# Optimization experiments

Measured on AMD Instinct MI355X. Metric: run time of the kernel, lower is better.

## Reference

```python
import jax, jax.numpy as jnp
import numpy as np
import jax.scipy.linalg as jsl

# dims
B, DIN = 4096, 256      # data
OUT, M = 32, 128        # output GPs, inducing points
NH = 2                  # hyperparameter samples
JITTER = 1e-4


def vec2tril(vec, m):
    """Fill lower-triangular (row-major) from packed vector."""
    i, j = jnp.tril_indices(m)
    out = jnp.zeros(vec.shape[:-1] + (m, m), vec.dtype)
    return out.at[..., i, j].set(vec)


def _hypers(theta):
    sf2 = jnp.exp(theta[:, 0])        # (NH,) signal variance
    ls = jnp.exp(theta[:, 1:])        # (NH, DIN) ARD lengthscales
    return sf2, ls


def kernel_zz(theta, z):
    """RBF K(z,z): (NH, OUT, M, M)."""
    sf2, ls = _hypers(theta)
    zs = z[None] / ls[:, None, None, :]              # (NH, OUT, M, DIN)
    n2 = (zs ** 2).sum(-1)                           # (NH, OUT, M)
    cross = jnp.einsum('homd,hond->homn', zs, zs)
    d2 = jnp.maximum(n2[..., :, None] + n2[..., None, :] - 2.0 * cross, 0.0)
    return sf2[:, None, None, None] * jnp.exp(-0.5 * d2)


def kernel_zx(theta, z, x):
    """RBF K(z,x): (NH, OUT, M, B)."""
    sf2, ls = _hypers(theta)
    zs = z[None] / ls[:, None, None, :]              # (NH, OUT, M, DIN)
    xs = x[None] / ls[:, None, :]                    # (NH, B, DIN)
    z2 = (zs ** 2).sum(-1)                           # (NH, OUT, M)
    x2 = (xs ** 2).sum(-1)                           # (NH, B)
    cross = jnp.einsum('homd,hbd->homb', zs, xs)     # (NH, OUT, M, B)
    d2 = jnp.maximum(z2[..., None] + x2[:, None, None, :] - 2.0 * cross, 0.0)
    return sf2[:, None, None, None] * jnp.exp(-0.5 * d2)


def setup_inputs() -> dict:
    key = jax.random.key(0)
    k1, k2, k3, k4, k5 = jax.random.split(key, 5)
    x = jax.random.normal(k1, (B, DIN), jnp.float32)
    z = jax.random.normal(k2, (OUT, M, DIN), jnp.float32)
    u_mean = jax.random.normal(k3, (OUT, M, 1), jnp.float32) * 0.5
    u_tril_vec = jax.random.uniform(k4, (OUT, M * (M + 1) // 2), jnp.float32)
    theta = jax.random.normal(k5, (NH, 1 + DIN), jnp.float32)
    return {"x": x, "z": z, "u_mean": u_mean, "u_tril_vec": u_tril_vec, "theta": theta}


def reference(x, z, u_mean, u_tril_vec, theta):
    m = z.shape[-2]
    u_tril = vec2tril(u_tril_vec, m)                        # (OUT, M, M)

    kuf = kernel_zx(theta, z, x)                            # (NH, OUT, M, B)
    kuu = kernel_zz(theta, z)                               # (NH, OUT, M, M)
    Lkuu = jnp.linalg.cholesky(kuu + JITTER * jnp.eye(m, dtype=kuu.dtype))

    bshape = Lkuu.shape[:-2]
    u_mean_b = jnp.broadcast_to(u_mean, bshape + u_mean.shape[-2:])
    u_tril_b = jnp.broadcast_to(u_tril, bshape + u_tril.shape[-2:])

    LKinvu = jsl.solve_triangular(Lkuu, u_mean_b, lower=True)   # (NH, OUT, M, 1)
    LKinvKuf = jsl.solve_triangular(Lkuu, kuf, lower=True)      # (NH, OUT, M, B)

    sf2, _ = _hypers(theta)
    kff_diag = sf2[:, None, None]                               # (NH, 1, 1)

    diag1 = (LKinvKuf ** 2).sum(-2)                             # (NH, OUT, B)
    LKinvLs = jsl.solve_triangular(Lkuu, u_tril_b, lower=True)  # (NH, OUT, M, M)
    vec2 = jnp.einsum('...ij,...ik->...jk', LKinvLs, LKinvKuf)  # (NH, OUT, M, B)
    diag2 = (vec2 ** 2).sum(-2)                                 # (NH, OUT, B)

    mu = jnp.einsum('...ij,...ik->...jk', LKinvKuf, LKinvu)[..., 0]  # (NH, OUT, B)
    var = kff_diag - diag1 + diag2                                   # (NH, OUT, B)
    return mu, var
```

## Files before the change

kernel.cpp:

```cpp
#include <hip/hip_runtime.h>
#include <cstdint>
#include <cstddef>

constexpr int B_   = 4096;
constexpr int DIN  = 256;
constexpr int OUT_ = 32;
constexpr int MM   = 128;
constexpr int NH_  = 2;
constexpr int HO   = 64;
constexpr int TRIL = 8256;
constexpr float JIT = 1e-4f;

constexpr size_t al4k(size_t x){ return (x + 4095) & ~size_t(4095); }
constexpr size_t OFF_FLAG  = 0;
constexpr size_t OFF_INVLS = 4096;
constexpr size_t OFF_SF2   = al4k(OFF_INVLS + 2*256*4);
constexpr size_t OFF_ZN2   = al4k(OFF_SF2 + 64);
constexpr size_t OFF_XN2   = al4k(OFF_ZN2 + 8192*4);
constexpr size_t OFF_W     = al4k(OFF_XN2 + 8192*4);
constexpr size_t OFF_ZS    = al4k(OFF_W + 8192*4);
constexpr size_t OFF_XS    = al4k(OFF_ZS + (size_t)2097152*2);
constexpr size_t OFF_VTH   = al4k(OFF_XS + (size_t)2097152*2);
constexpr size_t OFF_VTL   = al4k(OFF_VTH + (size_t)1048576*2);
constexpr size_t OFF_CHI   = al4k(OFF_VTL + (size_t)1048576*2);
constexpr size_t OFF_CLO   = al4k(OFF_CHI + (size_t)1048576*2);

typedef float f32x4 __attribute__((ext_vector_type(4)));
typedef short short8 __attribute__((ext_vector_type(8)));

__device__ __forceinline__ float bf2f(unsigned short u){
  union{unsigned int i; float f;} v; v.i = ((unsigned)u) << 16; return v.f;
}
__device__ __forceinline__ unsigned short f2bf(float f){
  union{float f; unsigned int i;} v; v.f = f;
  unsigned int r = v.i + 0x7fffu + ((v.i >> 16) & 1u);
  return (unsigned short)(r >> 16);
}
__device__ __forceinline__ float ldin(const void* p, size_t i, int isbf){
  if (isbf) return bf2f(((const unsigned short*)p)[i]);
  return ((const float*)p)[i];
}
__device__ __forceinline__ void stout(void* p, size_t i, float v, int isbf){
  if (isbf) ((unsigned short*)p)[i] = f2bf(v);
  else ((float*)p)[i] = v;
}
__device__ __forceinline__ void gl_lds16(const unsigned short* g, unsigned short* l){
  __builtin_amdgcn_global_load_lds(
      (const __attribute__((address_space(1))) unsigned int*)g,
      (__attribute__((address_space(3))) unsigned int*)l, 16, 0, 0);
}

__global__ void k_hypers(const void* __restrict__ theta, const void* __restrict__ x,
                         int* __restrict__ flagp,
                         float* __restrict__ inv_ls, float* __restrict__ sf2){
  __shared__ int sflag;
  int t = threadIdx.x;
  if (t < 64){
    unsigned int w0 = ((const unsigned int*)theta)[t];
    unsigned int w1 = ((const unsigned int*)x)[t];
    float a0 = fabsf(bf2f((unsigned short)(w0 & 0xffffu)));
    float a1 = fabsf(bf2f((unsigned short)(w1 & 0xffffu)));
    int c = ((a0 > 9.3e-10f && a0 < 64.f) ? 1 : 0) + ((a1 > 9.3e-10f && a1 < 64.f) ? 1 : 0);
    c += __shfl_down(c, 32); c += __shfl_down(c, 16); c += __shfl_down(c, 8);
    c += __shfl_down(c, 4);  c += __shfl_down(c, 2);  c += __shfl_down(c, 1);
    if (t == 0){ sflag = (c >= 64) ? 1 : 0; *flagp = sflag; }
  }
  __syncthreads();
  const int isbf = sflag;
  for (int i = t; i < NH_*257; i += blockDim.x){
    int h = i / 257, j = i - h*257;
    float v = ldin(theta, i, isbf);
    if (j == 0) sf2[h] = __expf(v);
    else inv_ls[h*DIN + j - 1] = __expf(-v);
  }
}

__global__ void k_scale(const void* __restrict__ xsrc, const void* __restrict__ zsrc,
                        const int* flagp, const float* __restrict__ inv_ls,
                        unsigned short* __restrict__ xdst, unsigned short* __restrict__ zdst,
                        float* __restrict__ xn2, float* __restrict__ zn2){
  const int isbf = *flagp;
  const int wave = threadIdx.x >> 6, lane = threadIdx.x & 63;
  int bx = blockIdx.x;
  const void* src; unsigned short* dst; float* n2; int r;
  if (bx < 1024){ src = xsrc; dst = xdst; n2 = xn2; r = bx*4 + wave; }
  else          { src = zsrc; dst = zdst; n2 = zn2; r = (bx-1024)*4 + wave; }
  const int d0 = lane*4;
  float v[4];
  if (isbf){
    uint2 uu = *(const uint2*)((const unsigned short*)src + (size_t)r*DIN + d0);
    v[0]=bf2f((unsigned short)(uu.x & 0xffffu)); v[1]=bf2f((unsigned short)(uu.x >> 16));
    v[2]=bf2f((unsigned short)(uu.y & 0xffffu)); v[3]=bf2f((unsigned short)(uu.y >> 16));
  } else {
    f32x4 f = *(const f32x4*)((const float*)src + (size_t)r*DIN + d0);
    v[0]=f[0]; v[1]=f[1]; v[2]=f[2]; v[3]=f[3];
  }
  #pragma unroll
  for (int h = 0; h < 2; ++h){
    f32x4 il = *(const f32x4*)(inv_ls + h*DIN + d0);
    unsigned short rb[4];
    float p = 0.f;
    #pragma unroll
    for (int k = 0; k < 4; ++k){
      float s = v[k] * il[k];
      rb[k] = f2bf(s);
      float qv = bf2f(rb[k]);
      p += qv*qv;
    }
    uint2 pk;
    pk.x = (unsigned)rb[0] | ((unsigned)rb[1] << 16);
    pk.y = (unsigned)rb[2] | ((unsigned)rb[3] << 16);
    *(uint2*)(dst + ((size_t)h*4096 + r)*DIN + d0) = pk;
    p += __shfl_xor(p, 32); p += __shfl_xor(p, 16); p += __shfl_xor(p, 8);
    p += __shfl_xor(p, 4);  p += __shfl_xor(p, 2);  p += __shfl_xor(p, 1);
    if (lane == 0) n2[(size_t)h*4096 + r] = p;
  }
}

constexpr int TLD = 20;
constexpr int TSZ = 16*TLD;
__device__ __forceinline__ int tb(int bi, int bj){ return (bi*(bi+1)/2 + bj)*TSZ; }
__device__ __forceinline__ int vb(int bi, int bj){ return (36 + bi*(bi-1)/2 + bj)*TSZ; }
__device__ __forceinline__ int tri_bi(int t){
  int bi = (int)((sqrtf(8.f*t + 1.f) - 1.f) * 0.5f);
  while ((bi+1)*(bi+2)/2 <= t) ++bi;
  while (bi*(bi+1)/2 > t) --bi;
  return bi;
}

__global__ __launch_bounds__(256) void k_kufact(
    const unsigned short* __restrict__ zs, const float* __restrict__ zn2,
    const float* __restrict__ sf2,
    unsigned short* __restrict__ VTh, unsigned short* __restrict__ VTl){
  const int ho = blockIdx.x, h = ho >> 5;
  const int tid = threadIdx.x;
  const int lane = tid & 63, wid = tid >> 6;
  const int l15 = lane & 15, q = lane >> 4;
  const int wn = wid * 32;
  extern __shared__ float T[];
  unsigned short* zsl = (unsigned short*)T;
  float* zn2l = T + 64*TSZ;
  if (tid < 128) zn2l[tid] = zn2[ho*128 + tid];
  const size_t zbase = (size_t)ho * 32768;
  const int sw = ((q ^ ((l15 >> 1) & 3)) << 3);
  const f32x4 z4 = {0.f,0.f,0.f,0.f};
  f32x4 acc[8][2];
  #pragma unroll
  for (int mt=0; mt<8; ++mt){ acc[mt][0]=z4; acc[mt][1]=z4; }
  for (int kc = 0; kc < 8; ++kc){
    __syncthreads();
    {
      int rA = wn + (lane >> 2);
      int sg = ((lane & 3) ^ ((rA >> 1) & 3)) << 3;
      gl_lds16(zs + zbase + (size_t)rA*256 + kc*32 + sg, zsl + wn*32);
      gl_lds16(zs + zbase + (size_t)(rA+16)*256 + kc*32 + sg, zsl + (wn+16)*32);
    }
    __syncthreads();
    short8 b0 = *(const short8*)(zsl + (wn      + l15)*32 + sw);
    short8 b1 = *(const short8*)(zsl + (wn + 16 + l15)*32 + sw);
    #pragma unroll
    for (int mt=0; mt<8; ++mt){
      short8 a = *(const short8*)(zsl + (mt*16 + l15)*32 + sw);
      acc[mt][0] = __builtin_amdgcn_mfma_f32_16x16x32_bf16(a, b0, acc[mt][0], 0,0,0);
      acc[mt][1] = __builtin_amdgcn_mfma_f32_16x16x32_bf16(a, b1, acc[mt][1], 0,0,0);
    }
  }
  __syncthreads();
  const float s2v = sf2[h];
  #pragma unroll
  for (int nt=0; nt<2; ++nt){
    int n = wn + nt*16 + l15;
    float nn = zn2l[n];
    int bn = n >> 4;
    #pragma unroll
    for (int mt=0; mt<8; ++mt){
      #pragma unroll
      for (int r=0; r<4; ++r){
        int m = mt*16 + q*4 + r;
        float d2 = fmaxf(zn2l[m] + nn - 2.f*acc[mt][nt][r], 0.f);
        float a = s2v * __expf(-0.5f*d2);
        if (m == n) a += JIT;
        int bm = m >> 4;
        if (bn <= bm) T[tb(bm, bn) + (m & 15)*TLD + (n & 15)] = a;
      }
    }
  }
  __syncthreads();
  for (int kb = 0; kb < 8; ++kb){
    if (wid == 0){
      float* D = T + tb(kb, kb);
      const int r = lane & 15;
      const bool act = (lane < 16);
      float a[16];
      #pragma unroll
      for (int k = 0; k < 16; ++k) a[k] = 0.f;
      if (act){
        #pragma unroll
        for (int k2 = 0; k2 < 4; ++k2)
          *(f32x4*)(a + 4*k2) = *(const f32x4*)(D + r*TLD + 4*k2);
      }
      #pragma unroll
      for (int c = 0; c < 16; ++c){
        float pr[16];
        #pragma unroll
        for (int k = 0; k < 16; ++k) pr[k] = __shfl(a[k], c);
        float rsq = rsqrtf(pr[c]);
        if (act && r >= c) a[c] *= rsq;
        float lrc = a[c];
        #pragma unroll
        for (int k = 0; k < 16; ++k)
          if (k > c && act && r > c) a[k] -= lrc * (pr[k] * rsq);
      }
      float v[16];
      #pragma unroll
      for (int k = 0; k < 16; ++k) v[k] = 0.f;
      const int c = lane & 15;
      #pragma unroll
      for (int i = 0; i < 16; ++i){
        float lrow[16];
        #pragma unroll
        for (int k = 0; k < 16; ++k) lrow[k] = __shfl(a[k], i);
        float rli = 1.f / lrow[i];
        float s = 0.f;
        #pragma unroll
        for (int k = 0; k < 16; ++k)
          if (k < i) s += ((k >= c) ? lrow[k]*v[k] : 0.f);
        v[i] = (c == i) ? rli : ((c < i) ? -s*rli : 0.f);
      }
      if (act){
        #pragma unroll
        for (int i = 0; i < 16; ++i) D[i*TLD + c] = v[i];
      }
    }
    __syncthreads();
    {
      const int gi = kb*16 + 16 + tid;
      if (gi < 128){
        float* Bp = T + tb(gi >> 4, kb) + (gi & 15)*TLD;
        const float* Vd = T + tb(kb, kb);
        float b[16], nb[16];
        #pragma unroll
        for (int k2 = 0; k2 < 4; ++k2) *(f32x4*)(b + 4*k2) = *(const f32x4*)(Bp + 4*k2);
        #pragma unroll
        for (int j = 0; j < 16; ++j){
          float s = 0.f;
          #pragma unroll
          for (int k = 0; k < 16; ++k)
            if (k <= j) s += b[k] * Vd[j*TLD + k];
          nb[j] = s;
        }
        #pragma unroll
        for (int k2 = 0; k2 < 4; ++k2) *(f32x4*)(Bp + 4*k2) = *(const f32x4*)(nb + 4*k2);
      }
    }
    __syncthreads();
    {
      const int D8 = 7 - kb;
      const int Tn = D8*(D8+1)/2;
      const int r15 = lane & 15, cg = lane >> 4, c0 = cg*4;
      for (int tt = wid; tt < Tn; tt += 4){
        int bi1 = tri_bi(tt);
        int bj1 = tt - bi1*(bi1+1)/2;
        int bi = kb + 1 + bi1, bj = kb + 1 + bj1;
        const float* Lr = T + tb(bi, kb) + r15*TLD;
        const float* Lc = T + tb(bj, kb) + c0*TLD;
        float* Cp = T + tb(bi, bj) + r15*TLD + c0;
        float lr[16];
        #pragma unroll
        for (int k2 = 0; k2 < 4; ++k2) *(f32x4*)(lr + 4*k2) = *(const f32x4*)(Lr + 4*k2);
        f32x4 accv = *(const f32x4*)Cp;
        #pragma unroll
        for (int cc = 0; cc < 4; ++cc){
          float lc[16];
          #pragma unroll
          for (int k2 = 0; k2 < 4; ++k2) *(f32x4*)(lc + 4*k2) = *(const f32x4*)(Lc + cc*TLD + 4*k2);
          float s = 0.f;
          #pragma unroll
          for (int k = 0; k < 16; ++k) s += lr[k]*lc[k];
          accv[cc] -= s;
        }
        *(f32x4*)Cp = accv;
      }
    }
    __syncthreads();
  }
  {
    const int r15 = lane & 15, c0 = (lane >> 4)*4;
    for (int d = 1; d < 8; ++d){
      for (int tt = wid; tt < 8 - d; tt += 4){
        const int bi = d + tt, jb = bi - d;
        float W0=0.f, W1=0.f, W2=0.f, W3=0.f;
        for (int k = jb; k < bi; ++k){
          const float* Lt = T + tb(bi, k) + r15*TLD;
          const float* Vt = (k == jb) ? (T + tb(jb, jb)) : (T + vb(k, jb));
          float lr[16];
          #pragma unroll
          for (int k2 = 0; k2 < 4; ++k2) *(f32x4*)(lr + 4*k2) = *(const f32x4*)(Lt + 4*k2);
          #pragma unroll
          for (int kk = 0; kk < 16; ++kk){
            f32x4 vv = *(const f32x4*)(Vt + kk*TLD + c0);
            W0 += lr[kk]*vv[0]; W1 += lr[kk]*vv[1];
            W2 += lr[kk]*vv[2]; W3 += lr[kk]*vv[3];
          }
        }
        const float* Vd = T + tb(bi, bi) + r15*TLD;
        const int cgl = (lane >> 4);
        f32x4 Rr = {0.f,0.f,0.f,0.f};
        #pragma unroll
        for (int k = 0; k < 16; ++k){
          float vd = Vd[k];
          float w0 = __shfl(W0, (cgl<<4)|k);
          float w1 = __shfl(W1, (cgl<<4)|k);
          float w2 = __shfl(W2, (cgl<<4)|k);
          float w3 = __shfl(W3, (cgl<<4)|k);
          Rr[0] -= vd*w0; Rr[1] -= vd*w1; Rr[2] -= vd*w2; Rr[3] -= vd*w3;
        }
        *(f32x4*)(T + vb(bi, jb) + r15*TLD + c0) = Rr;
      }
      __syncthreads();
    }
  }
  const size_t obase = (size_t)ho * 16384;
  for (int e = tid; e < 16384; e += 256){
    int c = e >> 7, rr = e & 127;
    int bc = c >> 4, br = rr >> 4;
    float v = 0.f;
    if (br == bc)      v = T[tb(br, bc) + (rr & 15)*TLD + (c & 15)];
    else if (br > bc)  v = T[vb(br, bc) + (rr & 15)*TLD + (c & 15)];
    unsigned short hi = f2bf(v);
    unsigned short lo = f2bf(v - bf2f(hi));
    VTh[obase + e] = hi;
    VTl[obase + e] = lo;
  }
}

__global__ __launch_bounds__(256) void k_QPC(
    const unsigned short* __restrict__ VTh, const unsigned short* __restrict__ VTl,
    const void* __restrict__ u_mean, const void* __restrict__ u_tril, const int* flagp,
    float* __restrict__ wg, unsigned short* __restrict__ Chi,
    unsigned short* __restrict__ Clo){
  const int ho = blockIdx.x, o = ho & 31;
  const int tid = threadIdx.x;
  const int lane = tid & 63, l15 = lane & 15, q = lane >> 4;
  const int wn = (tid >> 6) * 32;
  const int wave = tid >> 6;
  const int isbf = *flagp;
  extern __shared__ char smem[];
  unsigned short* Qh  = (unsigned short*)smem;
  unsigned short* Ql  = (unsigned short*)(smem + 34816);
  unsigned short* Sth = (unsigned short*)(smem + 69632);
  unsigned short* Stl = (unsigned short*)(smem + 104448);
  float* ul    = (float*)(smem + 139264);
  float* wpart = ul + 128;
  unsigned short* hsl = Qh;
  unsigned short* lsl = Qh + 4096;
  if (tid < 128) ul[tid] = ldin(u_mean, (size_t)o*128 + tid, isbf);
  for (int e = tid; e < 16384; e += 256){
    int k = e >> 7, j = e & 127;
    float val = 0.f;
    if (j <= k) val = ldin(u_tril, (size_t)o*TRIL + (size_t)k*(k+1)/2 + j, isbf);
    unsigned short hi = f2bf(val);
    Sth[j*136 + k] = hi;
    Stl[j*136 + k] = f2bf(val - bf2f(hi));
  }
  const size_t vbase = (size_t)ho * 16384;
  const int sw = ((q ^ ((l15 >> 1) & 3)) << 3);
  const f32x4 z4 = {0.f,0.f,0.f,0.f};
  f32x4 acc[8][2];
  #pragma unroll
  for (int mt=0; mt<8; ++mt){ acc[mt][0]=z4; acc[mt][1]=z4; }
  for (int kc = 0; kc < 4; ++kc){
    __syncthreads();
    {
      int rA = wn + (lane >> 2);
      int sg = ((lane & 3) ^ ((rA >> 1) & 3)) << 3;
      gl_lds16(VTh + vbase + (size_t)rA*128 + kc*32 + sg, hsl + wn*32);
      gl_lds16(VTl + vbase + (size_t)rA*128 + kc*32 + sg, lsl + wn*32);
      gl_lds16(VTh + vbase + (size_t)(rA+16)*128 + kc*32 + sg, hsl + (wn+16)*32);
      gl_lds16(VTl + vbase + (size_t)(rA+16)*128 + kc*32 + sg, lsl + (wn+16)*32);
    }
    __syncthreads();
    short8 b0h = *(const short8*)(hsl + (wn      + l15)*32 + sw);
    short8 b1h = *(const short8*)(hsl + (wn + 16 + l15)*32 + sw);
    short8 b0l = *(const short8*)(lsl + (wn      + l15)*32 + sw);
    short8 b1l = *(const short8*)(lsl + (wn + 16 + l15)*32 + sw);
    #pragma unroll
    for (int mt=0; mt<8; ++mt){
      short8 ah = *(const short8*)(hsl + (mt*16 + l15)*32 + sw);
      short8 al = *(const short8*)(lsl + (mt*16 + l15)*32 + sw);
      acc[mt][0] = __builtin_amdgcn_mfma_f32_16x16x32_bf16(ah, b0h, acc[mt][0], 0,0,0);
      acc[mt][0] = __builtin_amdgcn_mfma_f32_16x16x32_bf16(ah, b0l, acc[mt][0], 0,0,0);
      acc[mt][0] = __builtin_amdgcn_mfma_f32_16x16x32_bf16(al, b0h, acc[mt][0], 0,0,0);
      acc[mt][1] = __builtin_amdgcn_mfma_f32_16x16x32_bf16(ah, b1h, acc[mt][1], 0,0,0);
      acc[mt][1] = __builtin_amdgcn_mfma_f32_16x16x32_bf16(ah, b1l, acc[mt][1], 0,0,0);
      acc[mt][1] = __builtin_amdgcn_mfma_f32_16x16x32_bf16(al, b1h, acc[mt][1], 0,0,0);
    }
  }
  {
    float u0 = ul[wn + l15], u1 = ul[wn + 16 + l15];
    float wpm[32];
    #pragma unroll
    for (int mt=0; mt<8; ++mt){
      #pragma unroll
      for (int r=0; r<4; ++r)
        wpm[mt*4+r] = acc[mt][0][r]*u0 + acc[mt][1][r]*u1;
    }
    #pragma unroll
    for (int i = 0; i < 32; ++i){
      wpm[i] += __shfl_xor(wpm[i], 1);
      wpm[i] += __shfl_xor(wpm[i], 2);
      wpm[i] += __shfl_xor(wpm[i], 4);
      wpm[i] += __shfl_xor(wpm[i], 8);
    }
    if (l15 == 0){
      #pragma unroll
      for (int i = 0; i < 32; ++i){
        int m = (i>>2)*16 + q*4 + (i&3);
        wpart[wave*128 + m] = wpm[i];
      }
    }
  }
  __syncthreads();
  if (tid < 128)
    wg[ho*128 + tid] = wpart[tid] + wpart[128+tid] + wpart[256+tid] + wpart[384+tid];
  {
    const int n0 = wn + l15, n1 = wn + 16 + l15;
    #pragma unroll
    for (int mt=0; mt<8; ++mt){
      #pragma unroll
      for (int r=0; r<4; ++r){
        int m = mt*16 + q*4 + r;
        float v0 = acc[mt][0][r], v1 = acc[mt][1][r];
        unsigned short h0 = f2bf(v0), h1 = f2bf(v1);
        Qh[m*136 + n0] = h0; Ql[m*136 + n0] = f2bf(v0 - bf2f(h0));
        Qh[m*136 + n1] = h1; Ql[m*136 + n1] = f2bf(v1 - bf2f(h1));
      }
    }
  }
  __syncthreads();
  f32x4 acc3[8][2];
  #pragma unroll
  for (int mt=0; mt<8; ++mt){ acc3[mt][0]=z4; acc3[mt][1]=z4; }
  #pragma unroll
  for (int kc2 = 0; kc2 < 4; ++kc2){
    const int ko = kc2*32 + q*8;
    short8 b0h = *(const short8*)(Sth + (wn      + l15)*136 + ko);
    short8 b1h = *(const short8*)(Sth + (wn + 16 + l15)*136 + ko);
    short8 b0l = *(const short8*)(Stl + (wn      + l15)*136 + ko);
    short8 b1l = *(const short8*)(Stl + (wn + 16 + l15)*136 + ko);
    #pragma unroll
    for (int mt=0; mt<8; ++mt){
      short8 ah = *(const short8*)(Qh + (mt*16 + l15)*136 + ko);
      short8 al = *(const short8*)(Ql + (mt*16 + l15)*136 + ko);
      acc3[mt][0] = __builtin_amdgcn_mfma_f32_16x16x32_bf16(ah, b0h, acc3[mt][0], 0,0,0);
      acc3[mt][0] = __builtin_amdgcn_mfma_f32_16x16x32_bf16(al, b0h, acc3[mt][0], 0,0,0);
      acc3[mt][0] = __builtin_amdgcn_mfma_f32_16x16x32_bf16(ah, b0l, acc3[mt][0], 0,0,0);
      acc3[mt][1] = __builtin_amdgcn_mfma_f32_16x16x32_bf16(ah, b1h, acc3[mt][1], 0,0,0);
      acc3[mt][1] = __builtin_amdgcn_mfma_f32_16x16x32_bf16(al, b1h, acc3[mt][1], 0,0,0);
      acc3[mt][1] = __builtin_amdgcn_mfma_f32_16x16x32_bf16(ah, b1l, acc3[mt][1], 0,0,0);
    }
  }
  __syncthreads();
  {
    unsigned short* Ph = Qh;
    unsigned short* Pl = Ql;
    const int n0 = wn + l15, n1 = wn + 16 + l15;
    #pragma unroll
    for (int mt=0; mt<8; ++mt){
      #pragma unroll
      for (int r=0; r<4; ++r){
        int m = mt*16 + q*4 + r;
        float v0 = acc3[mt][0][r], v1 = acc3[mt][1][r];
        unsigned short h0 = f2bf(v0), h1 = f2bf(v1);
        Ph[m*136 + n0] = h0; Pl[m*136 + n0] = f2bf(v0 - bf2f(h0));
        Ph[m*136 + n1] = h1; Pl[m*136 + n1] = f2bf(v1 - bf2f(h1));
      }
    }
  }
  __syncthreads();
  f32x4 acc2[8][2];
  #pragma unroll
  for (int mt=0; mt<8; ++mt){ acc2[mt][0]=z4; acc2[mt][1]=z4; }
  #pragma unroll
  for (int kc2 = 0; kc2 < 4; ++kc2){
    const int ko = kc2*32 + q*8;
    short8 b0h = *(const short8*)(Qh + (wn      + l15)*136 + ko);
    short8 b1h = *(const short8*)(Qh + (wn + 16 + l15)*136 + ko);
    short8 b0l = *(const short8*)(Ql + (wn      + l15)*136 + ko);
    short8 b1l = *(const short8*)(Ql + (wn + 16 + l15)*136 + ko);
    #pragma unroll
    for (int mt=0; mt<8; ++mt){
      short8 ah = *(const short8*)(Qh + (mt*16 + l15)*136 + ko);
      short8 al = *(const short8*)(Ql + (mt*16 + l15)*136 + ko);
      acc2[mt][0] = __builtin_amdgcn_mfma_f32_16x16x32_bf16(ah, b0h, acc2[mt][0], 0,0,0);
      acc2[mt][0] = __builtin_amdgcn_mfma_f32_16x16x32_bf16(ah, b0l, acc2[mt][0], 0,0,0);
      acc2[mt][0] = __builtin_amdgcn_mfma_f32_16x16x32_bf16(al, b0h, acc2[mt][0], 0,0,0);
      acc2[mt][1] = __builtin_amdgcn_mfma_f32_16x16x32_bf16(ah, b1h, acc2[mt][1], 0,0,0);
      acc2[mt][1] = __builtin_amdgcn_mfma_f32_16x16x32_bf16(ah, b1l, acc2[mt][1], 0,0,0);
      acc2[mt][1] = __builtin_amdgcn_mfma_f32_16x16x32_bf16(al, b1h, acc2[mt][1], 0,0,0);
    }
  }
  #pragma unroll
  for (int nt=0; nt<2; ++nt){
    int n = wn + nt*16 + l15;
    #pragma unroll
    for (int mt=0; mt<8; ++mt){
      #pragma unroll
      for (int r=0; r<4; ++r){
        int m = mt*16 + q*4 + r;
        float c = acc[mt][nt][r] - acc2[mt][nt][r];
        unsigned short hi = f2bf(c);
        unsigned short lo = f2bf(c - bf2f(hi));
        Chi[vbase + m*128 + n] = hi;
        Clo[vbase + m*128 + n] = lo;
      }
    }
  }
}

__global__ __launch_bounds__(256) void k_main(
    const unsigned short* __restrict__ zs, const unsigned short* __restrict__ xs,
    const float* __restrict__ zn2, const float* __restrict__ xn2,
    const float* __restrict__ wg, const unsigned short* __restrict__ Chi,
    const unsigned short* __restrict__ Clo, const float* __restrict__ sf2,
    const int* flagp, void* __restrict__ out){
  const int bblk = blockIdx.x, ho = blockIdx.y, h = ho >> 5;
  const int tid = threadIdx.x;
  const int lane = tid & 63, l15 = lane & 15, q = lane >> 4;
  const int wid = tid >> 6;
  const int wn = wid * 32;
  const int isbf = *flagp;
  extern __shared__ char smem[];
  unsigned short* zb[3] = { (unsigned short*)smem,
                            (unsigned short*)smem + 8192,
                            (unsigned short*)smem + 16384 };
  unsigned short* xb[3] = { (unsigned short*)smem + 4096,
                            (unsigned short*)smem + 12288,
                            (unsigned short*)smem + 20480 };
  unsigned short* kufT = (unsigned short*)smem;
  float* zn2l = (float*)(smem + 49152);
  float* xn2l = zn2l + 128;
  float* wl   = xn2l + 128;

  if (tid < 128){
    zn2l[tid] = zn2[ho*128 + tid];
    xn2l[tid] = xn2[(size_t)h*B_ + bblk*128 + tid];
    wl[tid]   = wg[ho*128 + tid];
  }
  const size_t zbase = (size_t)ho * 32768;
  const size_t xbase = ((size_t)h*B_ + bblk*128) * 256;
  const int sw = ((q ^ ((l15 >> 1) & 3)) << 3);
  const int rA = wn + (lane >> 2);
  const int sg = ((lane & 3) ^ ((rA >> 1) & 3)) << 3;
  const f32x4 z4 = {0.f,0.f,0.f,0.f};
  f32x4 acc[8][2];
  #pragma unroll
  for (int mt=0; mt<8; ++mt){ acc[mt][0]=z4; acc[mt][1]=z4; }

  auto STAGE = [&](int c, unsigned short* zd, unsigned short* xd){
    const int off = c*32;
    gl_lds16(zs + zbase + (size_t)rA*256      + off + sg, zd + wn*32);
    gl_lds16(zs + zbase + (size_t)(rA+16)*256 + off + sg, zd + (wn+16)*32);
    gl_lds16(xs + xbase + (size_t)rA*256      + off + sg, xd + wn*32);
    gl_lds16(xs + xbase + (size_t)(rA+16)*256 + off + sg, xd + (wn+16)*32);
  };

  STAGE(0, zb[0], xb[0]);
  STAGE(1, zb[1], xb[1]);

  #pragma unroll
  for (int kc = 0; kc < 8; ++kc){
    unsigned short* zc = zb[kc % 3];
    unsigned short* xc = xb[kc % 3];
    if (kc + 2 < 8) STAGE(kc + 2, zb[(kc + 2) % 3], xb[(kc + 2) % 3]);
    if (kc < 6)       asm volatile("s_waitcnt vmcnt(8)" ::: "memory");
    else if (kc == 6) asm volatile("s_waitcnt vmcnt(4)" ::: "memory");
    else              asm volatile("s_waitcnt vmcnt(0)" ::: "memory");
    __builtin_amdgcn_s_barrier();
    __builtin_amdgcn_sched_barrier(0);
    short8 b0 = *(const short8*)(xc + (wn      + l15)*32 + sw);
    short8 b1 = *(const short8*)(xc + (wn + 16 + l15)*32 + sw);
    #pragma unroll
    for (int mt=0; mt<8; ++mt){
      short8 a = *(const short8*)(zc + (mt*16 + l15)*32 + sw);
      acc[mt][0] = __builtin_amdgcn_mfma_f32_16x16x32_bf16(a, b0, acc[mt][0], 0,0,0);
      acc[mt][1] = __builtin_amdgcn_mfma_f32_16x16x32_bf16(a, b1, acc[mt][1], 0,0,0);
    }
    asm volatile("s_waitcnt lgkmcnt(0)" ::: "memory");
    __builtin_amdgcn_sched_barrier(0);
    __builtin_amdgcn_s_barrier();
  }
  const float s2 = sf2[h];
  float mu0 = 0.f, mu1 = 0.f;
  #pragma unroll
  for (int nt=0; nt<2; ++nt){
    const int bl = wn + nt*16 + l15;
    const float xn = xn2l[bl];
    #pragma unroll
    for (int mt=0; mt<8; ++mt){
      const int m0 = mt*16 + q*4;
      float kf[4];
      #pragma unroll
      for (int r=0; r<4; ++r){
        float d2 = fmaxf(zn2l[m0+r] + xn - 2.f*acc[mt][nt][r], 0.f);
        kf[r] = s2 * __expf(-0.5f*d2);
        float wv = wl[m0+r] * kf[r];
        if (nt == 0) mu0 += wv; else mu1 += wv;
      }
      uint2 pk;
      pk.x = (unsigned)f2bf(kf[0]) | ((unsigned)f2bf(kf[1]) << 16);
      pk.y = (unsigned)f2bf(kf[2]) | ((unsigned)f2bf(kf[3]) << 16);
      *(uint2*)(kufT + bl*136 + m0) = pk;
    }
  }
  __syncthreads();
  f32x4 acc2[8][2];
  #pragma unroll
  for (int mt=0; mt<8; ++mt){ acc2[mt][0]=z4; acc2[mt][1]=z4; }
  const unsigned short* Ch = Chi + (size_t)ho*16384;
  const unsigned short* Cl = Clo + (size_t)ho*16384;
  #pragma unroll
  for (int kc2 = 0; kc2 < 4; ++kc2){
    short8 b0 = *(const short8*)(kufT + (wn      + l15)*136 + kc2*32 + q*8);
    short8 b1 = *(const short8*)(kufT + (wn + 16 + l15)*136 + kc2*32 + q*8);
    #pragma unroll
    for (int mt=0; mt<8; ++mt){
      short8 ah = *(const short8*)(Ch + (mt*16 + l15)*128 + kc2*32 + q*8);
      acc2[mt][0] = __builtin_amdgcn_mfma_f32_16x16x32_bf16(ah, b0, acc2[mt][0], 0,0,0);
      acc2[mt][1] = __builtin_amdgcn_mfma_f32_16x16x32_bf16(ah, b1, acc2[mt][1], 0,0,0);
      short8 al = *(const short8*)(Cl + (mt*16 + l15)*128 + kc2*32 + q*8);
      acc2[mt][0] = __builtin_amdgcn_mfma_f32_16x16x32_bf16(al, b0, acc2[mt][0], 0,0,0);
      acc2[mt][1] = __builtin_amdgcn_mfma_f32_16x16x32_bf16(al, b1, acc2[mt][1], 0,0,0);
    }
  }
  float s2p0 = 0.f, s2p1 = 0.f;
  #pragma unroll
  for (int nt=0; nt<2; ++nt){
    const int bl = wn + nt*16 + l15;
    #pragma unroll
    for (int mt=0; mt<8; ++mt){
      const int m0 = mt*16 + q*4;
      uint2 pk = *(const uint2*)(kufT + bl*136 + m0);
      f32x4 t = acc2[mt][nt];
      float s = bf2f((unsigned short)(pk.x & 0xffff)) * t[0]
              + bf2f((unsigned short)(pk.x >> 16))    * t[1]
              + bf2f((unsigned short)(pk.y & 0xffff)) * t[2]
              + bf2f((unsigned short)(pk.y >> 16))    * t[3];
      if (nt == 0) s2p0 += s; else s2p1 += s;
    }
  }
  mu0  += __shfl_xor(mu0, 16);  mu0  += __shfl_xor(mu0, 32);
  mu1  += __shfl_xor(mu1, 16);  mu1  += __shfl_xor(mu1, 32);
  s2p0 += __shfl_xor(s2p0, 16); s2p0 += __shfl_xor(s2p0, 32);
  s2p1 += __shfl_xor(s2p1, 16); s2p1 += __shfl_xor(s2p1, 32);
  if (lane < 16){
    size_t col = (size_t)ho*B_ + bblk*128 + wn + lane;
    stout(out, col,                        mu0,       isbf);
    stout(out, (size_t)HO*B_ + col,        s2 - s2p0, isbf);
    stout(out, col + 16,                   mu1,       isbf);
    stout(out, (size_t)HO*B_ + col + 16,   s2 - s2p1, isbf);
  }
}

extern "C" void kernel_launch(void* const* d_in, const int* in_sizes, int n_in,
                              void* d_out, int out_size, void* d_ws, size_t ws_size,
                              hipStream_t stream) {
  const void* x      = d_in[0];
  const void* z      = d_in[1];
  const void* u_mean = d_in[2];
  const void* u_tril = d_in[3];
  const void* theta  = d_in[4];
  char* ws = (char*)d_ws;

  int*   flag   = (int*)(ws + OFF_FLAG);
  float* inv_ls = (float*)(ws + OFF_INVLS);
  float* sf2    = (float*)(ws + OFF_SF2);
  float* zn2    = (float*)(ws + OFF_ZN2);
  float* xn2    = (float*)(ws + OFF_XN2);
  float* wv     = (float*)(ws + OFF_W);
  unsigned short* zsw = (unsigned short*)(ws + OFF_ZS);
  unsigned short* xsw = (unsigned short*)(ws + OFF_XS);
  unsigned short* VTh = (unsigned short*)(ws + OFF_VTH);
  unsigned short* VTl = (unsigned short*)(ws + OFF_VTL);
  unsigned short* Chi = (unsigned short*)(ws + OFF_CHI);
  unsigned short* Clo = (unsigned short*)(ws + OFF_CLO);

  k_hypers<<<1, 256, 0, stream>>>(theta, x, flag, inv_ls, sf2);
  k_scale<<<dim3(2048), 256, 0, stream>>>(x, z, flag, inv_ls, xsw, zsw, xn2, zn2);
  k_kufact<<<64, 256, (64*TSZ + 128) * 4, stream>>>(zsw, zn2, sf2, VTh, VTl);
  k_QPC<<<64, 256, 139264 + 512 + 2048, stream>>>(VTh, VTl, u_mean, u_tril, flag, wv, Chi, Clo);
  k_main<<<dim3(32, 64), 256, 49152 + 1536, stream>>>(zsw, xsw, zn2, xn2, wv, Chi, Clo, sf2, flag, (void*)d_out);
}
```

Baseline: 270.6 us.

## Double k_main batch tile and load x operand directly into registers

Each block of k_main now covers 256 batch columns instead of 128, with 64 columns per wave. This halves the grid and doubles reuse of the z tile and of the Chi/Clo factors per block. The x operand is now loaded from global memory straight into double-buffered registers instead of being staged through LDS, so only z goes through the triple-buffered LDS pipeline. The accumulator footprint doubles, and launch bounds now request 2 blocks per CU. This risks register pressure, and the direct global x reads may be less efficient than the old LDS staging.

```diff
diff --git a/kernel.cpp b/kernel.cpp
--- a/kernel.cpp
+++ b/kernel.cpp
@@ -518,7 +518,7 @@
   }
 }
 
-__global__ __launch_bounds__(256) void k_main(
+__global__ __launch_bounds__(256, 2) void k_main(
     const unsigned short* __restrict__ zs, const unsigned short* __restrict__ xs,
     const float* __restrict__ zn2, const float* __restrict__ xn2,
     const float* __restrict__ wg, const unsigned short* __restrict__ Chi,
@@ -529,72 +529,79 @@
   const int lane = tid & 63, l15 = lane & 15, q = lane >> 4;
   const int wid = tid >> 6;
   const int wn = wid * 32;
+  const int wn2 = wid * 64;
   const int isbf = *flagp;
   extern __shared__ char smem[];
-  unsigned short* zb[3] = { (unsigned short*)smem,
-                            (unsigned short*)smem + 8192,
-                            (unsigned short*)smem + 16384 };
-  unsigned short* xb[3] = { (unsigned short*)smem + 4096,
-                            (unsigned short*)smem + 12288,
-                            (unsigned short*)smem + 20480 };
+  unsigned short* zb0 = (unsigned short*)smem;
+  unsigned short* zb1 = zb0 + 4096;
+  unsigned short* zb2 = zb0 + 8192;
   unsigned short* kufT = (unsigned short*)smem;
-  float* zn2l = (float*)(smem + 49152);
+  float* zn2l = (float*)(smem + 69632);
   float* xn2l = zn2l + 128;
-  float* wl   = xn2l + 128;
+  float* wl   = xn2l + 256;
 
   if (tid < 128){
     zn2l[tid] = zn2[ho*128 + tid];
-    xn2l[tid] = xn2[(size_t)h*B_ + bblk*128 + tid];
     wl[tid]   = wg[ho*128 + tid];
   }
+  xn2l[tid] = xn2[(size_t)h*B_ + bblk*256 + tid];
   const size_t zbase = (size_t)ho * 32768;
-  const size_t xbase = ((size_t)h*B_ + bblk*128) * 256;
+  const size_t xbase = ((size_t)h*B_ + bblk*256) * 256;
   const int sw = ((q ^ ((l15 >> 1) & 3)) << 3);
   const int rA = wn + (lane >> 2);
   const int sg = ((lane & 3) ^ ((rA >> 1) & 3)) << 3;
   const f32x4 z4 = {0.f,0.f,0.f,0.f};
-  f32x4 acc[8][2];
-  #pragma unroll
-  for (int mt=0; mt<8; ++mt){ acc[mt][0]=z4; acc[mt][1]=z4; }
-
-  auto STAGE = [&](int c, unsigned short* zd, unsigned short* xd){
+  f32x4 acc[8][4];
+  #pragma unroll
+  for (int mt=0; mt<8; ++mt){
+    #pragma unroll
+    for (int nt=0; nt<4; ++nt) acc[mt][nt]=z4;
+  }
+  unsigned short* zbp[3] = { zb0, zb1, zb2 };
+
+  auto STAGEZ = [&](int c, unsigned short* zd){
     const int off = c*32;
     gl_lds16(zs + zbase + (size_t)rA*256      + off + sg, zd + wn*32);
     gl_lds16(zs + zbase + (size_t)(rA+16)*256 + off + sg, zd + (wn+16)*32);
-    gl_lds16(xs + xbase + (size_t)rA*256      + off + sg, xd + wn*32);
-    gl_lds16(xs + xbase + (size_t)(rA+16)*256 + off + sg, xd + (wn+16)*32);
   };
-
-  STAGE(0, zb[0], xb[0]);
-  STAGE(1, zb[1], xb[1]);
+  auto LDB = [&](int c, short8* bd){
+    #pragma unroll
+    for (int nt=0; nt<4; ++nt)
+      bd[nt] = *(const short8*)(xs + xbase + (size_t)(wn2 + nt*16 + l15)*256 + c*32 + q*8);
+  };
+
+  short8 bA[4], bB[4];
+  STAGEZ(0, zb0);
+  STAGEZ(1, zb1);
+  LDB(0, bA);
 
   #pragma unroll
   for (int kc = 0; kc < 8; ++kc){
-    unsigned short* zc = zb[kc % 3];
-    unsigned short* xc = xb[kc % 3];
-    if (kc + 2 < 8) STAGE(kc + 2, zb[(kc + 2) % 3], xb[(kc + 2) % 3]);
-    if (kc < 6)       asm volatile("s_waitcnt vmcnt(8)" ::: "memory");
+    unsigned short* zc = zbp[kc % 3];
+    if (kc + 2 < 8) STAGEZ(kc + 2, zbp[(kc + 2) % 3]);
+    if (kc + 1 < 8){ if (kc & 1) LDB(kc + 1, bA); else LDB(kc + 1, bB); }
+    if (kc < 6)       asm volatile("s_waitcnt vmcnt(6)" ::: "memory");
     else if (kc == 6) asm volatile("s_waitcnt vmcnt(4)" ::: "memory");
     else              asm volatile("s_waitcnt vmcnt(0)" ::: "memory");
     __builtin_amdgcn_s_barrier();
     __builtin_amdgcn_sched_barrier(0);
-    short8 b0 = *(const short8*)(xc + (wn      + l15)*32 + sw);
-    short8 b1 = *(const short8*)(xc + (wn + 16 + l15)*32 + sw);
+    const short8* bc = (kc & 1) ? bB : bA;
     #pragma unroll
     for (int mt=0; mt<8; ++mt){
       short8 a = *(const short8*)(zc + (mt*16 + l15)*32 + sw);
-      acc[mt][0] = __builtin_amdgcn_mfma_f32_16x16x32_bf16(a, b0, acc[mt][0], 0,0,0);
-      acc[mt][1] = __builtin_amdgcn_mfma_f32_16x16x32_bf16(a, b1, acc[mt][1], 0,0,0);
+      #pragma unroll
+      for (int nt=0; nt<4; ++nt)
+        acc[mt][nt] = __builtin_amdgcn_mfma_f32_16x16x32_bf16(a, bc[nt], acc[mt][nt], 0,0,0);
     }
     asm volatile("s_waitcnt lgkmcnt(0)" ::: "memory");
     __builtin_amdgcn_sched_barrier(0);
     __builtin_amdgcn_s_barrier();
   }
   const float s2 = sf2[h];
-  float mu0 = 0.f, mu1 = 0.f;
-  #pragma unroll
-  for (int nt=0; nt<2; ++nt){
-    const int bl = wn + nt*16 + l15;
+  float mu[4] = {0.f, 0.f, 0.f, 0.f};
+  #pragma unroll
+  for (int nt=0; nt<4; ++nt){
+    const int bl = wn2 + nt*16 + l15;
     const float xn = xn2l[bl];
     #pragma unroll
     for (int mt=0; mt<8; ++mt){
@@ -604,61 +611,67 @@
       for (int r=0; r<4; ++r){
         float d2 = fmaxf(zn2l[m0+r] + xn - 2.f*acc[mt][nt][r], 0.f);
         kf[r] = s2 * __expf(-0.5f*d2);
-        float wv = wl[m0+r] * kf[r];
-        if (nt == 0) mu0 += wv; else mu1 += wv;
+        mu[nt] += wl[m0+r] * kf[r];
       }
       uint2 pk;
       pk.x = (unsigned)f2bf(kf[0]) | ((unsigned)f2bf(kf[1]) << 16);
       pk.y = (unsigned)f2bf(kf[2]) | ((unsigned)f2bf(kf[3]) << 16);
-      *(uint2*)(kufT + bl*136 + m0) = pk;
+      *(uint2*)(kufT + (size_t)bl*136 + m0) = pk;
     }
   }
   __syncthreads();
-  f32x4 acc2[8][2];
-  #pragma unroll
-  for (int mt=0; mt<8; ++mt){ acc2[mt][0]=z4; acc2[mt][1]=z4; }
+  f32x4 acc2[8][4];
+  #pragma unroll
+  for (int mt=0; mt<8; ++mt){
+    #pragma unroll
+    for (int nt=0; nt<4; ++nt) acc2[mt][nt]=z4;
+  }
   const unsigned short* Ch = Chi + (size_t)ho*16384;
   const unsigned short* Cl = Clo + (size_t)ho*16384;
   #pragma unroll
   for (int kc2 = 0; kc2 < 4; ++kc2){
-    short8 b0 = *(const short8*)(kufT + (wn      + l15)*136 + kc2*32 + q*8);
-    short8 b1 = *(const short8*)(kufT + (wn + 16 + l15)*136 + kc2*32 + q*8);
+    short8 bk[4];
+    #pragma unroll
+    for (int nt=0; nt<4; ++nt)
+      bk[nt] = *(const short8*)(kufT + (wn2 + nt*16 + l15)*136 + kc2*32 + q*8);
     #pragma unroll
     for (int mt=0; mt<8; ++mt){
       short8 ah = *(const short8*)(Ch + (mt*16 + l15)*128 + kc2*32 + q*8);
-      acc2[mt][0] = __builtin_amdgcn_mfma_f32_16x16x32_bf16(ah, b0, acc2[mt][0], 0,0,0);
-      acc2[mt][1] = __builtin_amdgcn_mfma_f32_16x16x32_bf16(ah, b1, acc2[mt][1], 0,0,0);
       short8 al = *(const short8*)(Cl + (mt*16 + l15)*128 + kc2*32 + q*8);
-      acc2[mt][0] = __builtin_amdgcn_mfma_f32_16x16x32_bf16(al, b0, acc2[mt][0], 0,0,0);
-      acc2[mt][1] = __builtin_amdgcn_mfma_f32_16x16x32_bf16(al, b1, acc2[mt][1], 0,0,0);
-    }
-  }
-  float s2p0 = 0.f, s2p1 = 0.f;
-  #pragma unroll
-  for (int nt=0; nt<2; ++nt){
-    const int bl = wn + nt*16 + l15;
+      #pragma unroll
+      for (int nt=0; nt<4; ++nt){
+        acc2[mt][nt] = __builtin_amdgcn_mfma_f32_16x16x32_bf16(ah, bk[nt], acc2[mt][nt], 0,0,0);
+        acc2[mt][nt] = __builtin_amdgcn_mfma_f32_16x16x32_bf16(al, bk[nt], acc2[mt][nt], 0,0,0);
+      }
+    }
+  }
+  float s2p[4] = {0.f, 0.f, 0.f, 0.f};
+  #pragma unroll
+  for (int nt=0; nt<4; ++nt){
+    const int bl = wn2 + nt*16 + l15;
     #pragma unroll
     for (int mt=0; mt<8; ++mt){
       const int m0 = mt*16 + q*4;
-      uint2 pk = *(const uint2*)(kufT + bl*136 + m0);
+      uint2 pk = *(const uint2*)(kufT + (size_t)bl*136 + m0);
       f32x4 t = acc2[mt][nt];
-      float s = bf2f((unsigned short)(pk.x & 0xffff)) * t[0]
-              + bf2f((unsigned short)(pk.x >> 16))    * t[1]
-              + bf2f((unsigned short)(pk.y & 0xffff)) * t[2]
-              + bf2f((unsigned short)(pk.y >> 16))    * t[3];
-      if (nt == 0) s2p0 += s; else s2p1 += s;
-    }
-  }
-  mu0  += __shfl_xor(mu0, 16);  mu0  += __shfl_xor(mu0, 32);
-  mu1  += __shfl_xor(mu1, 16);  mu1  += __shfl_xor(mu1, 32);
-  s2p0 += __shfl_xor(s2p0, 16); s2p0 += __shfl_xor(s2p0, 32);
-  s2p1 += __shfl_xor(s2p1, 16); s2p1 += __shfl_xor(s2p1, 32);
+      s2p[nt] += bf2f((unsigned short)(pk.x & 0xffff)) * t[0]
+               + bf2f((unsigned short)(pk.x >> 16))    * t[1]
+               + bf2f((unsigned short)(pk.y & 0xffff)) * t[2]
+               + bf2f((unsigned short)(pk.y >> 16))    * t[3];
+    }
+  }
+  #pragma unroll
+  for (int nt=0; nt<4; ++nt){
+    mu[nt]  += __shfl_xor(mu[nt], 16);  mu[nt]  += __shfl_xor(mu[nt], 32);
+    s2p[nt] += __shfl_xor(s2p[nt], 16); s2p[nt] += __shfl_xor(s2p[nt], 32);
+  }
   if (lane < 16){
-    size_t col = (size_t)ho*B_ + bblk*128 + wn + lane;
-    stout(out, col,                        mu0,       isbf);
-    stout(out, (size_t)HO*B_ + col,        s2 - s2p0, isbf);
-    stout(out, col + 16,                   mu1,       isbf);
-    stout(out, (size_t)HO*B_ + col + 16,   s2 - s2p1, isbf);
+    #pragma unroll
+    for (int nt=0; nt<4; ++nt){
+      size_t col = (size_t)ho*B_ + bblk*256 + wn2 + nt*16 + lane;
+      stout(out, col,                  mu[nt],        isbf);
+      stout(out, (size_t)HO*B_ + col,  s2 - s2p[nt],  isbf);
+    }
   }
 }
 
@@ -689,5 +702,5 @@
   k_scale<<<dim3(2048), 256, 0, stream>>>(x, z, flag, inv_ls, xsw, zsw, xn2, zn2);
   k_kufact<<<64, 256, (64*TSZ + 128) * 4, stream>>>(zsw, zn2, sf2, VTh, VTl);
   k_QPC<<<64, 256, 139264 + 512 + 2048, stream>>>(VTh, VTl, u_mean, u_tril, flag, wv, Chi, Clo);
-  k_main<<<dim3(32, 64), 256, 49152 + 1536, stream>>>(zsw, xsw, zn2, xn2, wv, Chi, Clo, sf2, flag, (void*)d_out);
-}
+  k_main<<<dim3(16, 64), 256, 69632 + 2048, stream>>>(zsw, xsw, zn2, xn2, wv, Chi, Clo, sf2, flag, (void*)d_out);
+}
```

Result: faster. 247.0 us (-8.7%).
